# Optimization experiments

Hardware: AMD Instinct MI355X
Metric: run time of the kernel (lower is better)

The kernel has to match this reference:

```python
import jax, jax.numpy as jnp
import numpy as np

N, E, D, H = 50000, 800000, 128, 128
LN_EPS = 1e-3  # keras LayerNormalization default epsilon


def layer_norm(x, g, b):
    mu = jnp.mean(x, axis=-1, keepdims=True)
    var = jnp.mean(jnp.square(x - mu), axis=-1, keepdims=True)
    return (x - mu) * jax.lax.rsqrt(var + LN_EPS) * g + b


def mlp3(x, W1, b1, W2, b2, W3, b3, g1, be1, g2, be2):
    # 3-layer MLP: two hidden layers (relu + layernorm), linear output head
    h = layer_norm(jax.nn.relu(x @ W1 + b1), g1, be1)
    h = layer_norm(jax.nn.relu(h @ W2 + b2), g2, be2)
    return h @ W3 + b3


def _dense_init(key, fan_in, fan_out):
    return jax.random.normal(key, (fan_in, fan_out), jnp.float32) / np.sqrt(fan_in)


def setup_inputs() -> dict:
    key = jax.random.key(0)
    ks = jax.random.split(key, 12)
    query = jax.random.normal(ks[0], (N, D), jnp.float32)
    memory = jax.random.normal(ks[1], (N, D), jnp.float32)
    row = jnp.sort(jax.random.randint(ks[2], (E,), 0, N, jnp.int32))
    col = jax.random.randint(ks[3], (E,), 0, N, jnp.int32)
    # pre_process MLP: input 2D -> H -> H -> 1 (heads=1)
    pW1 = _dense_init(ks[4], 2 * D, H); pb1 = jnp.zeros((H,), jnp.float32)
    pW2 = _dense_init(ks[5], H, H);     pb2 = jnp.zeros((H,), jnp.float32)
    pW3 = _dense_init(ks[6], H, 1);     pb3 = jnp.zeros((1,), jnp.float32)
    pg1 = jnp.ones((H,), jnp.float32);  pbe1 = jnp.zeros((H,), jnp.float32)
    pg2 = jnp.ones((H,), jnp.float32);  pbe2 = jnp.zeros((H,), jnp.float32)
    # memory MLP: D -> H -> H -> H
    mW1 = _dense_init(ks[7], D, H); mb1 = jnp.zeros((H,), jnp.float32)
    mW2 = _dense_init(ks[8], H, H); mb2 = jnp.zeros((H,), jnp.float32)
    mW3 = _dense_init(ks[9], H, H); mb3 = jnp.zeros((H,), jnp.float32)
    mg1 = jnp.ones((H,), jnp.float32); mbe1 = jnp.zeros((H,), jnp.float32)
    mg2 = jnp.ones((H,), jnp.float32); mbe2 = jnp.zeros((H,), jnp.float32)
    return dict(query=query, memory=memory, row=row, col=col,
                pW1=pW1, pb1=pb1, pW2=pW2, pb2=pb2, pW3=pW3, pb3=pb3,
                pg1=pg1, pbe1=pbe1, pg2=pg2, pbe2=pbe2,
                mW1=mW1, mb1=mb1, mW2=mW2, mb2=mb2, mW3=mW3, mb3=mb3,
                mg1=mg1, mbe1=mbe1, mg2=mg2, mbe2=mbe2)


def reference(query, memory, row, col,
              pW1, pb1, pW2, pb2, pW3, pb3, pg1, pbe1, pg2, pbe2,
              mW1, mb1, mW2, mb2, mW3, mb3, mg1, mbe1, mg2, mbe2):
    # per-edge gather of query (target) and memory (source) node features
    units = jnp.concatenate([query[row], memory[col]], axis=-1)  # [E, 2D]
    h = jnp.tanh(mlp3(units, pW1, pb1, pW2, pb2, pW3, pb3, pg1, pbe1, pg2, pbe2))[:, 0]  # [E]
    mem_head = mlp3(memory, mW1, mb1, mW2, mb2, mW3, mb3, mg1, mbe1, mg2, mbe2)  # [N, H]
    # sparse_dense_matmul: out[i] = sum_{edges (i,j)} h_e * mem_head[j]
    out = jax.ops.segment_sum(h[:, None] * mem_head[col], row, num_segments=N)  # [N, H]
    return out
```

## Files before the change

kernel.cpp:

```cpp
#include <hip/hip_runtime.h>
#include <hip/hip_bf16.h>

typedef __attribute__((ext_vector_type(8))) short  svec8;
typedef __attribute__((ext_vector_type(4))) short  svec4;
typedef __attribute__((ext_vector_type(8))) __bf16 bfvec8;
typedef __attribute__((ext_vector_type(4))) float  f32x4;
typedef __attribute__((ext_vector_type(2))) float  f32x2;
typedef __attribute__((ext_vector_type(4))) unsigned uvec4;

#define LN_EPS 1e-3f

__device__ __forceinline__ short f2bf(float f) {
  union { float f; unsigned u; } v; v.f = f;
  unsigned u = v.u;
  u += 0x7fff + ((u >> 16) & 1);
  return (short)(u >> 16);
}

__device__ __forceinline__ unsigned pk2(float a, float b) {
  unsigned short ua = __builtin_bit_cast(unsigned short, (__bf16)a);
  unsigned short ub = __builtin_bit_cast(unsigned short, (__bf16)b);
  return (unsigned)ua | ((unsigned)ub << 16);
}

__device__ __forceinline__ f32x2 up2(unsigned w) {
  f32x2 r;
  r[0] = __builtin_bit_cast(float, w << 16);
  r[1] = __builtin_bit_cast(float, w & 0xffff0000u);
  return r;
}

__device__ __forceinline__ f32x4 mfma16(svec8 a, svec8 b, f32x4 c) {
  return __builtin_amdgcn_mfma_f32_16x16x32_bf16(
      __builtin_bit_cast(bfvec8, a), __builtin_bit_cast(bfvec8, b), c, 0, 0, 0);
}

__global__ __launch_bounds__(256) void setup_kernel(
    const float* __restrict__ pW1, const float* __restrict__ pW2,
    const float* __restrict__ pg1,
    const float* __restrict__ mW1, const float* __restrict__ mW2,
    const float* __restrict__ mW3,
    short* __restrict__ w1qp, short* __restrict__ w1mp,
    short* __restrict__ w2p,  short* __restrict__ mw1p,
    short* __restrict__ mw2p, short* __restrict__ mw3p,
    const int* __restrict__ row, int E, int N, int* __restrict__ off,
    const float* __restrict__ g1, const float* __restrict__ be1,
    const float* __restrict__ b2, const float* __restrict__ g2,
    const float* __restrict__ w3, const float* __restrict__ be2,
    const float* __restrict__ b3,
    float* __restrict__ s2, float* __restrict__ b2pv,
    float* __restrict__ gw, float* __restrict__ consts, int nboff)
{
  const int b = blockIdx.x;
  const int tid = threadIdx.x;
  if (b < 384) {
    int idx = b * 256 + tid;
    int which = idx >> 14, p = idx & 16383;
    int j = p & 7, lane = (p >> 3) & 63, t = p >> 9;
    int nf = t & 7, ks = t >> 3;
    int k = ks * 32 + (lane >> 4) * 8 + j;
    int n = nf * 16 + (lane & 15);
    const float* src; short* dst; float scale = 1.f;
    switch (which) {
      case 0:  src = pW1;         dst = w1qp; break;
      case 1:  src = pW1 + 16384; dst = w1mp; break;
      case 2:  src = pW2;         dst = w2p; scale = pg1[k]; break;
      case 3:  src = mW1;         dst = mw1p; break;
      case 4:  src = mW2;         dst = mw2p; break;
      default: src = mW3;         dst = mw3p; break;
    }
    dst[p] = f2bf(scale * src[k * 128 + n]);
  } else if (b < 384 + nboff) {
    int i = (b - 384) * 256 + tid;
    if (i > N) return;
    int lo = 0, hi = E;
    while (lo < hi) { int mid = (lo + hi) >> 1; if (row[mid] < i) lo = mid + 1; else hi = mid; }
    off[i] = lo;
  } else {
    __shared__ float tmp[256];
    int n = tid;
    if (n < 128) {
      float s = 0.f, bb = 0.f;
      for (int k = 0; k < 128; ++k) {
        float w = pW2[k * 128 + n];
        s  = fmaf(g1[k],  w, s);
        bb = fmaf(be1[k], w, bb);
      }
      s2[n]   = s;
      b2pv[n] = bb + b2[n];
      float g = g2[n] * w3[n];
      gw[n] = g;
      tmp[n]       = g;
      tmp[128 + n] = be2[n] * w3[n];
    }
    __syncthreads();
    if (n == 0) {
      float a = 0.f, c = 0.f;
      for (int i = 0; i < 128; ++i) { a += tmp[i]; c += tmp[128 + i]; }
      consts[0] = a;
      consts[1] = c + b3[0];
    }
  }
}

__global__ __launch_bounds__(256) void node_kernel(
    const float* __restrict__ mem, const float* __restrict__ query,
    const short* __restrict__ w1p, const short* __restrict__ w2p, const short* __restrict__ w3p,
    const short* __restrict__ wmp, const short* __restrict__ wqp,
    const float* __restrict__ b1v, const float* __restrict__ b2v, const float* __restrict__ b3v,
    const float* __restrict__ g1v, const float* __restrict__ be1v,
    const float* __restrict__ g2v, const float* __restrict__ be2v,
    const float* __restrict__ pb1,
    short* __restrict__ mhb, short* __restrict__ mwt, short* __restrict__ qwt,
    int N, int nbm)
{
  __shared__ short Xs[64 * 128];
  __shared__ short H1s[64 * 128];
  __shared__ float redA[4][64];
  __shared__ float redB[4][64];

  const int tid  = threadIdx.x;
  const int wv   = tid >> 6;
  const int lane = tid & 63;
  const int g16  = lane >> 4;
  const int l16  = lane & 15;
  const bool is_mem = (blockIdx.x < nbm);
  const int r0   = (is_mem ? blockIdx.x : blockIdx.x - nbm) * 64;
  const float* src = is_mem ? mem : query;

  #pragma unroll
  for (int it = 0; it < 8; ++it) {
    int c = tid + it * 256;
    int r = c >> 5;
    int part = c & 31;
    int gr = r0 + r; if (gr >= N) gr = N - 1;
    f32x4 v = *(const f32x4*)(src + (size_t)gr * 128 + part * 4);
    svec4 s;
    s[0] = f2bf(v[0]); s[1] = f2bf(v[1]); s[2] = f2bf(v[2]); s[3] = f2bf(v[3]);
    int b = (r * 256 + part * 8) ^ ((r & 7) << 4);
    *(svec4*)((char*)Xs + b) = s;
  }
  __syncthreads();

  const int nfb = wv * 2;
  const int col0 = wv * 32 + l16, col1 = col0 + 16;

  if (!is_mem) {
    f32x4 acc[4][2];
    #pragma unroll
    for (int mf = 0; mf < 4; ++mf) { f32x4 z = {0.f,0.f,0.f,0.f}; acc[mf][0] = z; acc[mf][1] = z; }
    #pragma unroll
    for (int ks = 0; ks < 4; ++ks) {
      svec8 bw0 = *(const svec8*)(wqp + (((ks * 8 + nfb + 0) * 64 + lane) << 3));
      svec8 bw1 = *(const svec8*)(wqp + (((ks * 8 + nfb + 1) * 64 + lane) << 3));
      #pragma unroll
      for (int mf = 0; mf < 4; ++mf) {
        int row = mf * 16 + l16;
        int byt = (row * 256 + ks * 64 + g16 * 16) ^ ((row & 7) << 4);
        svec8 a = *(const svec8*)((const char*)Xs + byt);
        acc[mf][0] = mfma16(a, bw0, acc[mf][0]);
        acc[mf][1] = mfma16(a, bw1, acc[mf][1]);
      }
    }
    float bi0 = pb1[col0], bi1 = pb1[col1];
    #pragma unroll
    for (int mf = 0; mf < 4; ++mf)
      #pragma unroll
      for (int r = 0; r < 4; ++r) {
        int rr = mf * 16 + g16 * 4 + r;
        int gr = r0 + rr;
        if (gr < N) {
          qwt[(size_t)gr * 128 + col0] = f2bf(acc[mf][0][r] + bi0);
          qwt[(size_t)gr * 128 + col1] = f2bf(acc[mf][1][r] + bi1);
        }
      }
    return;
  }

  f32x4 acc[4][2], accm[4][2];
  #pragma unroll
  for (int mf = 0; mf < 4; ++mf) {
    f32x4 z = {0.f,0.f,0.f,0.f};
    acc[mf][0] = z; acc[mf][1] = z; accm[mf][0] = z; accm[mf][1] = z;
  }
  #pragma unroll
  for (int ks = 0; ks < 4; ++ks) {
    svec8 bw0 = *(const svec8*)(w1p + (((ks * 8 + nfb + 0) * 64 + lane) << 3));
    svec8 bw1 = *(const svec8*)(w1p + (((ks * 8 + nfb + 1) * 64 + lane) << 3));
    svec8 bm0 = *(const svec8*)(wmp + (((ks * 8 + nfb + 0) * 64 + lane) << 3));
    svec8 bm1 = *(const svec8*)(wmp + (((ks * 8 + nfb + 1) * 64 + lane) << 3));
    #pragma unroll
    for (int mf = 0; mf < 4; ++mf) {
      int row = mf * 16 + l16;
      int byt = (row * 256 + ks * 64 + g16 * 16) ^ ((row & 7) << 4);
      svec8 a = *(const svec8*)((const char*)Xs + byt);
      acc[mf][0]  = mfma16(a, bw0, acc[mf][0]);
      acc[mf][1]  = mfma16(a, bw1, acc[mf][1]);
      accm[mf][0] = mfma16(a, bm0, accm[mf][0]);
      accm[mf][1] = mfma16(a, bm1, accm[mf][1]);
    }
  }
  #pragma unroll
  for (int mf = 0; mf < 4; ++mf)
    #pragma unroll
    for (int r = 0; r < 4; ++r) {
      int rr = mf * 16 + g16 * 4 + r;
      int gr = r0 + rr;
      if (gr < N) {
        mwt[(size_t)gr * 128 + col0] = f2bf(accm[mf][0][r]);
        mwt[(size_t)gr * 128 + col1] = f2bf(accm[mf][1][r]);
      }
    }

  float bi0 = b1v[col0], bi1 = b1v[col1];
  float ga0 = g1v[col0], ga1 = g1v[col1];
  float bb0 = be1v[col0], bb1 = be1v[col1];
  float y[4][2][4], ps[4][4], pq[4][4];
  #pragma unroll
  for (int mf = 0; mf < 4; ++mf)
    #pragma unroll
    for (int r = 0; r < 4; ++r) {
      float y0 = fmaxf(acc[mf][0][r] + bi0, 0.f);
      float y1 = fmaxf(acc[mf][1][r] + bi1, 0.f);
      y[mf][0][r] = y0; y[mf][1][r] = y1;
      ps[mf][r] = y0 + y1;
      pq[mf][r] = y0 * y0 + y1 * y1;
    }
  #pragma unroll
  for (int mk = 1; mk <= 8; mk <<= 1)
    #pragma unroll
    for (int mf = 0; mf < 4; ++mf)
      #pragma unroll
      for (int r = 0; r < 4; ++r) {
        ps[mf][r] += __shfl_xor(ps[mf][r], mk, 64);
        pq[mf][r] += __shfl_xor(pq[mf][r], mk, 64);
      }
  if (l16 == 0) {
    #pragma unroll
    for (int mf = 0; mf < 4; ++mf)
      #pragma unroll
      for (int r = 0; r < 4; ++r) {
        redA[wv][mf * 16 + g16 * 4 + r] = ps[mf][r];
        redB[wv][mf * 16 + g16 * 4 + r] = pq[mf][r];
      }
  }
  __syncthreads();
  #pragma unroll
  for (int mf = 0; mf < 4; ++mf)
    #pragma unroll
    for (int r = 0; r < 4; ++r) {
      int rr = mf * 16 + g16 * 4 + r;
      float s = redA[0][rr] + redA[1][rr] + redA[2][rr] + redA[3][rr];
      float q = redB[0][rr] + redB[1][rr] + redB[2][rr] + redB[3][rr];
      float mu = s * (1.f / 128.f);
      float var = fmaxf(q * (1.f / 128.f) - mu * mu, 0.f);
      float rstd = rsqrtf(var + LN_EPS);
      float z0 = (y[mf][0][r] - mu) * rstd * ga0 + bb0;
      float z1 = (y[mf][1][r] - mu) * rstd * ga1 + bb1;
      int by0 = (rr * 256 + col0 * 2) ^ ((rr & 7) << 4);
      int by1 = (rr * 256 + col1 * 2) ^ ((rr & 7) << 4);
      *(short*)((char*)H1s + by0) = f2bf(z0);
      *(short*)((char*)H1s + by1) = f2bf(z1);
    }
  __syncthreads();

  f32x4 acc2[4][2];
  #pragma unroll
  for (int mf = 0; mf < 4; ++mf) { f32x4 z = {0.f,0.f,0.f,0.f}; acc2[mf][0] = z; acc2[mf][1] = z; }
  #pragma unroll
  for (int ks = 0; ks < 4; ++ks) {
    svec8 bw0 = *(const svec8*)(w2p + (((ks * 8 + nfb + 0) * 64 + lane) << 3));
    svec8 bw1 = *(const svec8*)(w2p + (((ks * 8 + nfb + 1) * 64 + lane) << 3));
    #pragma unroll
    for (int mf = 0; mf < 4; ++mf) {
      int row = mf * 16 + l16;
      int byt = (row * 256 + ks * 64 + g16 * 16) ^ ((row & 7) << 4);
      svec8 a = *(const svec8*)((const char*)H1s + byt);
      acc2[mf][0] = mfma16(a, bw0, acc2[mf][0]);
      acc2[mf][1] = mfma16(a, bw1, acc2[mf][1]);
    }
  }

  float bi20 = b2v[col0], bi21 = b2v[col1];
  float ga20 = g2v[col0], ga21 = g2v[col1];
  float bb20 = be2v[col0], bb21 = be2v[col1];
  float y2[4][2][4];
  #pragma unroll
  for (int mf = 0; mf < 4; ++mf)
    #pragma unroll
    for (int r = 0; r < 4; ++r) {
      float y0 = fmaxf(acc2[mf][0][r] + bi20, 0.f);
      float y1 = fmaxf(acc2[mf][1][r] + bi21, 0.f);
      y2[mf][0][r] = y0; y2[mf][1][r] = y1;
      ps[mf][r] = y0 + y1;
      pq[mf][r] = y0 * y0 + y1 * y1;
    }
  #pragma unroll
  for (int mk = 1; mk <= 8; mk <<= 1)
    #pragma unroll
    for (int mf = 0; mf < 4; ++mf)
      #pragma unroll
      for (int r = 0; r < 4; ++r) {
        ps[mf][r] += __shfl_xor(ps[mf][r], mk, 64);
        pq[mf][r] += __shfl_xor(pq[mf][r], mk, 64);
      }
  if (l16 == 0) {
    #pragma unroll
    for (int mf = 0; mf < 4; ++mf)
      #pragma unroll
      for (int r = 0; r < 4; ++r) {
        redA[wv][mf * 16 + g16 * 4 + r] = ps[mf][r];
        redB[wv][mf * 16 + g16 * 4 + r] = pq[mf][r];
      }
  }
  __syncthreads();
  #pragma unroll
  for (int mf = 0; mf < 4; ++mf)
    #pragma unroll
    for (int r = 0; r < 4; ++r) {
      int rr = mf * 16 + g16 * 4 + r;
      float s = redA[0][rr] + redA[1][rr] + redA[2][rr] + redA[3][rr];
      float q = redB[0][rr] + redB[1][rr] + redB[2][rr] + redB[3][rr];
      float mu = s * (1.f / 128.f);
      float var = fmaxf(q * (1.f / 128.f) - mu * mu, 0.f);
      float rstd = rsqrtf(var + LN_EPS);
      float z0 = (y2[mf][0][r] - mu) * rstd * ga20 + bb20;
      float z1 = (y2[mf][1][r] - mu) * rstd * ga21 + bb21;
      int by0 = (rr * 256 + col0 * 2) ^ ((rr & 7) << 4);
      int by1 = (rr * 256 + col1 * 2) ^ ((rr & 7) << 4);
      *(short*)((char*)Xs + by0) = f2bf(z0);
      *(short*)((char*)Xs + by1) = f2bf(z1);
    }
  __syncthreads();

  f32x4 acc3[4][2];
  #pragma unroll
  for (int mf = 0; mf < 4; ++mf) { f32x4 z = {0.f,0.f,0.f,0.f}; acc3[mf][0] = z; acc3[mf][1] = z; }
  #pragma unroll
  for (int ks = 0; ks < 4; ++ks) {
    svec8 bw0 = *(const svec8*)(w3p + (((ks * 8 + nfb + 0) * 64 + lane) << 3));
    svec8 bw1 = *(const svec8*)(w3p + (((ks * 8 + nfb + 1) * 64 + lane) << 3));
    #pragma unroll
    for (int mf = 0; mf < 4; ++mf) {
      int row = mf * 16 + l16;
      int byt = (row * 256 + ks * 64 + g16 * 16) ^ ((row & 7) << 4);
      svec8 a = *(const svec8*)((const char*)Xs + byt);
      acc3[mf][0] = mfma16(a, bw0, acc3[mf][0]);
      acc3[mf][1] = mfma16(a, bw1, acc3[mf][1]);
    }
  }
  float bi30 = b3v[col0], bi31 = b3v[col1];
  #pragma unroll
  for (int mf = 0; mf < 4; ++mf)
    #pragma unroll
    for (int r = 0; r < 4; ++r) {
      int rr = mf * 16 + g16 * 4 + r;
      int gr = r0 + rr;
      if (gr < N) {
        mhb[(size_t)gr * 128 + col0] = f2bf(acc3[mf][0][r] + bi30);
        mhb[(size_t)gr * 128 + col1] = f2bf(acc3[mf][1][r] + bi31);
      }
    }
}

__device__ __forceinline__ void relu_stats(const svec8* qv, const svec8* mv,
                                           svec8* yf, float& ps_o, float& pq_o) {
  f32x2 psv = {0.f, 0.f}, pqv = {0.f, 0.f};
  #pragma unroll
  for (int ks2 = 0; ks2 < 4; ++ks2) {
    uvec4 qu = __builtin_bit_cast(uvec4, qv[ks2]);
    uvec4 mu = __builtin_bit_cast(uvec4, mv[ks2]);
    uvec4 u;
    #pragma unroll
    for (int p = 0; p < 4; ++p) {
      f32x2 y = __builtin_elementwise_max(up2(qu[p]) + up2(mu[p]), (f32x2){0.f, 0.f});
      psv += y;
      pqv += y * y;
      u[p] = pk2(y[0], y[1]);
    }
    yf[ks2] = __builtin_bit_cast(svec8, u);
  }
  float ps = psv[0] + psv[1], pq = pqv[0] + pqv[1];
  ps += __shfl_xor(ps, 16, 64); pq += __shfl_xor(pq, 16, 64);
  ps += __shfl_xor(ps, 32, 64); pq += __shfl_xor(pq, 32, 64);
  ps_o = ps; pq_o = pq;
}

__device__ __forceinline__ void epilogue(const f32x4* acc2, float rstd1, float mu1,
    const float* s2v, const float* b2pv, const float* gwv, float Sgw, float cb,
    float* __restrict__ hout, int e, bool valid, int lane, int g) {
  f32x2 rst = {rstd1, rstd1};
  f32x2 nmu = {-rstd1 * mu1, -rstd1 * mu1};
  f32x2 psv = {0.f,0.f}, pqv = {0.f,0.f}, pwv = {0.f,0.f};
  #pragma unroll
  for (int nf = 0; nf < 8; ++nf) {
    f32x4 s2 = *(const f32x4*)(s2v  + nf * 16 + g * 4);
    f32x4 bb = *(const f32x4*)(b2pv + nf * 16 + g * 4);
    f32x4 gw = *(const f32x4*)(gwv  + nf * 16 + g * 4);
    #pragma unroll
    for (int p = 0; p < 2; ++p) {
      f32x2 a   = { acc2[nf][2*p], acc2[nf][2*p+1] };
      f32x2 s2p = { s2[2*p], s2[2*p+1] };
      f32x2 bbp = { bb[2*p], bb[2*p+1] };
      f32x2 gwp = { gw[2*p], gw[2*p+1] };
      f32x2 h = rst * a + (nmu * s2p + bbp);
      f32x2 y = __builtin_elementwise_max(h, (f32x2){0.f, 0.f});
      psv += y;
      pqv += y * y;
      pwv += y * gwp;
    }
  }
  float ps2 = psv[0] + psv[1], pq2 = pqv[0] + pqv[1], pw2 = pwv[0] + pwv[1];
  ps2 += __shfl_xor(ps2, 16, 64); pq2 += __shfl_xor(pq2, 16, 64); pw2 += __shfl_xor(pw2, 16, 64);
  ps2 += __shfl_xor(ps2, 32, 64); pq2 += __shfl_xor(pq2, 32, 64); pw2 += __shfl_xor(pw2, 32, 64);
  float mu2   = ps2 * (1.f / 128.f);
  float var2  = fmaxf(pq2 * (1.f / 128.f) - mu2 * mu2, 0.f);
  float rstd2 = rsqrtf(var2 + LN_EPS);
  float p3 = fmaf(rstd2, pw2 - mu2 * Sgw, cb);
  if (lane < 16 && valid) hout[e] = tanhf(p3);
}

__global__ __launch_bounds__(256, 3) void edge_mlp_kernel(
    const short* __restrict__ qwt, const short* __restrict__ mwt,
    const int* __restrict__ rowi, const int* __restrict__ coli,
    const short* __restrict__ w2p,
    const float* __restrict__ s2v, const float* __restrict__ b2pv,
    const float* __restrict__ gwv, const float* __restrict__ consts,
    float* __restrict__ hout, int E)
{
  __shared__ short w2s[16384];

  const int tid  = threadIdx.x;
  const int wv   = tid >> 6;
  const int lane = tid & 63;
  const int g    = lane >> 4;
  const int l16  = lane & 15;

  const int nb  = gridDim.x;
  const int q8  = nb >> 3, r8 = nb & 7;
  const int xcd = blockIdx.x & 7, sub = blockIdx.x >> 3;
  const int bid = (xcd < r8 ? xcd * (q8 + 1) : r8 * (q8 + 1) + (xcd - r8) * q8) + sub;

  #pragma unroll
  for (int it = 0; it < 8; ++it) {
    int o = (it * 256 + tid) * 8;
    *(f32x4*)(w2s + o) = *(const f32x4*)(w2p + o);
  }
  __syncthreads();

  const int eb = bid * 128 + wv * 32;
  const int e0 = eb + l16, e1 = eb + 16 + l16;
  const bool v0 = (e0 < E), v1 = (e1 < E);
  const int ee0 = v0 ? e0 : 0, ee1 = v1 ? e1 : 0;
  const short* q0 = qwt + (size_t)rowi[ee0] * 128 + g * 8;
  const short* m0 = mwt + (size_t)coli[ee0] * 128 + g * 8;
  const short* q1 = qwt + (size_t)rowi[ee1] * 128 + g * 8;
  const short* m1 = mwt + (size_t)coli[ee1] * 128 + g * 8;

  svec8 qv0[4], mv0[4], qv1[4], mv1[4];
  #pragma unroll
  for (int ks2 = 0; ks2 < 4; ++ks2) {
    qv0[ks2] = *(const svec8*)(q0 + ks2 * 32);
    mv0[ks2] = *(const svec8*)(m0 + ks2 * 32);
    qv1[ks2] = *(const svec8*)(q1 + ks2 * 32);
    mv1[ks2] = *(const svec8*)(m1 + ks2 * 32);
  }

  svec8 yf0[4], yf1[4];
  float ps0, pq0, ps1, pq1;
  relu_stats(qv0, mv0, yf0, ps0, pq0);
  relu_stats(qv1, mv1, yf1, ps1, pq1);
  float mu1_0   = ps0 * (1.f / 128.f);
  float rstd1_0 = rsqrtf(fmaxf(pq0 * (1.f / 128.f) - mu1_0 * mu1_0, 0.f) + LN_EPS);
  float mu1_1   = ps1 * (1.f / 128.f);
  float rstd1_1 = rsqrtf(fmaxf(pq1 * (1.f / 128.f) - mu1_1 * mu1_1, 0.f) + LN_EPS);

  f32x4 acc2a[8], acc2b[8];
  #pragma unroll
  for (int nf = 0; nf < 8; ++nf) { f32x4 z = {0.f,0.f,0.f,0.f}; acc2a[nf] = z; acc2b[nf] = z; }
  __builtin_amdgcn_s_setprio(1);
  #pragma unroll
  for (int ks2 = 0; ks2 < 4; ++ks2) {
    #pragma unroll
    for (int nf = 0; nf < 8; ++nf) {
      svec8 w = *(const svec8*)(w2s + (((ks2 * 8 + nf) * 64 + lane) << 3));
      acc2a[nf] = mfma16(w, yf0[ks2], acc2a[nf]);
      acc2b[nf] = mfma16(w, yf1[ks2], acc2b[nf]);
    }
  }
  __builtin_amdgcn_s_setprio(0);

  float Sgw = consts[0], cb = consts[1];
  epilogue(acc2a, rstd1_0, mu1_0, s2v, b2pv, gwv, Sgw, cb, hout, e0, v0, lane, g);
  epilogue(acc2b, rstd1_1, mu1_1, s2v, b2pv, gwv, Sgw, cb, hout, e1, v1, lane, g);
}

__global__ __launch_bounds__(256) void segsum_kernel(
    const int* __restrict__ off, const int* __restrict__ coli,
    const float* __restrict__ hbuf, const short* __restrict__ mhb,
    float* __restrict__ out, int N)
{
  int wv = threadIdx.x >> 6, lane = threadIdx.x & 63;
  int i = blockIdx.x * 4 + wv;
  if (i >= N) return;
  int s = __builtin_amdgcn_readfirstlane(off[i]);
  int e = __builtin_amdgcn_readfirstlane(off[i + 1]);
  f32x2 acc = {0.f, 0.f};
  int k = s;
  for (; k + 8 <= e; k += 8) {
    float h[8]; unsigned w[8];
    #pragma unroll
    for (int u = 0; u < 8; ++u) {
      h[u] = hbuf[k + u];
      w[u] = *(const unsigned*)(mhb + (size_t)coli[k + u] * 128 + lane * 2);
    }
    #pragma unroll
    for (int u = 0; u < 8; ++u)
      acc += (f32x2){h[u], h[u]} * up2(w[u]);
  }
  for (; k < e; ++k) {
    float h = hbuf[k];
    unsigned w = *(const unsigned*)(mhb + (size_t)coli[k] * 128 + lane * 2);
    acc += (f32x2){h, h} * up2(w);
  }
  *(f32x2*)(out + (size_t)i * 128 + lane * 2) = acc;
}

extern "C" void kernel_launch(void* const* d_in, const int* in_sizes, int n_in,
                              void* d_out, int out_size, void* d_ws, size_t ws_size,
                              hipStream_t stream) {
  const float* query = (const float*)d_in[0];
  const float* mem   = (const float*)d_in[1];
  const int*   row   = (const int*)d_in[2];
  const int*   col   = (const int*)d_in[3];
  const float* pW1 = (const float*)d_in[4];  const float* pb1 = (const float*)d_in[5];
  const float* pW2 = (const float*)d_in[6];  const float* pb2 = (const float*)d_in[7];
  const float* pW3 = (const float*)d_in[8];  const float* pb3 = (const float*)d_in[9];
  const float* pg1 = (const float*)d_in[10]; const float* pbe1 = (const float*)d_in[11];
  const float* pg2 = (const float*)d_in[12]; const float* pbe2 = (const float*)d_in[13];
  const float* mW1 = (const float*)d_in[14]; const float* mb1 = (const float*)d_in[15];
  const float* mW2 = (const float*)d_in[16]; const float* mb2 = (const float*)d_in[17];
  const float* mW3 = (const float*)d_in[18]; const float* mb3 = (const float*)d_in[19];
  const float* mg1 = (const float*)d_in[20]; const float* mbe1 = (const float*)d_in[21];
  const float* mg2 = (const float*)d_in[22]; const float* mbe2 = (const float*)d_in[23];

  const int N = in_sizes[0] / 128;
  const int E = in_sizes[2];

  char* ws = (char*)d_ws;
  short* w1qp = (short*)(ws + 0);
  short* w1mp = (short*)(ws + 32768);
  short* w2p  = (short*)(ws + 65536);
  short* mw1p = (short*)(ws + 98304);
  short* mw2p = (short*)(ws + 131072);
  short* mw3p = (short*)(ws + 163840);
  float* s2v  = (float*)(ws + 196608);
  float* b2pv = (float*)(ws + 197120);
  float* gwv  = (float*)(ws + 197632);
  float* cons = (float*)(ws + 198144);
  int*   offs = (int*)(ws + 198208);
  size_t o = 198208 + (((size_t)(N + 1) * 4 + 255) / 256) * 256;
  short* qwt  = (short*)(ws + o);  o += (size_t)N * 128 * 2;
  short* mwt  = (short*)(ws + o);  o += (size_t)N * 128 * 2;
  short* mhb  = (short*)(ws + o);  o += (size_t)N * 128 * 2;
  float* hbuf = (float*)(ws + o);  o += (size_t)E * 4;

  if (ws_size < o) return;

  const int nboff = (N + 1 + 255) / 256;
  setup_kernel<<<384 + nboff + 1, 256, 0, stream>>>(
      pW1, pW2, pg1, mW1, mW2, mW3, w1qp, w1mp, w2p, mw1p, mw2p, mw3p,
      row, E, N, offs,
      pg1, pbe1, pb2, pg2, pW3, pbe2, pb3, s2v, b2pv, gwv, cons, nboff);

  const int nbm = (N + 63) / 64;
  node_kernel<<<2 * nbm, 256, 0, stream>>>(
      mem, query, mw1p, mw2p, mw3p, w1mp, w1qp,
      mb1, mb2, mb3, mg1, mbe1, mg2, mbe2, pb1,
      mhb, mwt, qwt, N, nbm);

  edge_mlp_kernel<<<(E + 127) / 128, 256, 0, stream>>>(
      qwt, mwt, row, col, w2p, s2v, b2pv, gwv, cons, hbuf, E);

  segsum_kernel<<<(N + 3) / 4, 256, 0, stream>>>(offs, col, hbuf, mhb, (float*)d_out, N);
}
```

Baseline: 179.0 us.

## Give each wave a private 16-row tile in the node MLP kernel

The node MLP kernel now has each wave own 16 full rows across all 128 output columns, instead of four waves sharing a 64-row tile split by columns. Inputs are loaded straight from global memory into MFMA A-fragments, and LayerNorm statistics are reduced entirely with in-wave shuffles. This removes the shared staging tile, the cross-wave reduction arrays and every __syncthreads. In exchange, each wave now loads the full weight matrices itself, which raises weight traffic from cache, and it holds more accumulators in registers.

```diff
diff --git a/kernel.cpp b/kernel.cpp
--- a/kernel.cpp
+++ b/kernel.cpp
@@ -114,253 +114,185 @@
     short* __restrict__ mhb, short* __restrict__ mwt, short* __restrict__ qwt,
     int N, int nbm)
 {
-  __shared__ short Xs[64 * 128];
-  __shared__ short H1s[64 * 128];
-  __shared__ float redA[4][64];
-  __shared__ float redB[4][64];
+  __shared__ char Hs[4][4096];
 
   const int tid  = threadIdx.x;
   const int wv   = tid >> 6;
   const int lane = tid & 63;
-  const int g16  = lane >> 4;
+  const int g    = lane >> 4;
   const int l16  = lane & 15;
   const bool is_mem = (blockIdx.x < nbm);
-  const int r0   = (is_mem ? blockIdx.x : blockIdx.x - nbm) * 64;
+  const int r0   = (is_mem ? blockIdx.x : blockIdx.x - nbm) * 64 + wv * 16;
   const float* src = is_mem ? mem : query;
 
-  #pragma unroll
-  for (int it = 0; it < 8; ++it) {
-    int c = tid + it * 256;
-    int r = c >> 5;
-    int part = c & 31;
-    int gr = r0 + r; if (gr >= N) gr = N - 1;
-    f32x4 v = *(const f32x4*)(src + (size_t)gr * 128 + part * 4);
-    svec4 s;
-    s[0] = f2bf(v[0]); s[1] = f2bf(v[1]); s[2] = f2bf(v[2]); s[3] = f2bf(v[3]);
-    int b = (r * 256 + part * 8) ^ ((r & 7) << 4);
-    *(svec4*)((char*)Xs + b) = s;
-  }
-  __syncthreads();
-
-  const int nfb = wv * 2;
-  const int col0 = wv * 32 + l16, col1 = col0 + 16;
+  int grow = r0 + l16; if (grow >= N) grow = N - 1;
+  const float* xrow = src + (size_t)grow * 128 + g * 8;
+  svec8 xf[4];
+  #pragma unroll
+  for (int ks = 0; ks < 4; ++ks) {
+    f32x4 a = *(const f32x4*)(xrow + ks * 32);
+    f32x4 b = *(const f32x4*)(xrow + ks * 32 + 4);
+    uvec4 u;
+    u[0] = pk2(a[0], a[1]); u[1] = pk2(a[2], a[3]);
+    u[2] = pk2(b[0], b[1]); u[3] = pk2(b[2], b[3]);
+    xf[ks] = __builtin_bit_cast(svec8, u);
+  }
 
   if (!is_mem) {
-    f32x4 acc[4][2];
-    #pragma unroll
-    for (int mf = 0; mf < 4; ++mf) { f32x4 z = {0.f,0.f,0.f,0.f}; acc[mf][0] = z; acc[mf][1] = z; }
-    #pragma unroll
-    for (int ks = 0; ks < 4; ++ks) {
-      svec8 bw0 = *(const svec8*)(wqp + (((ks * 8 + nfb + 0) * 64 + lane) << 3));
-      svec8 bw1 = *(const svec8*)(wqp + (((ks * 8 + nfb + 1) * 64 + lane) << 3));
+    f32x4 acc[8];
+    #pragma unroll
+    for (int nf = 0; nf < 8; ++nf) { f32x4 z = {0.f,0.f,0.f,0.f}; acc[nf] = z; }
+    #pragma unroll
+    for (int ks = 0; ks < 4; ++ks)
       #pragma unroll
-      for (int mf = 0; mf < 4; ++mf) {
-        int row = mf * 16 + l16;
-        int byt = (row * 256 + ks * 64 + g16 * 16) ^ ((row & 7) << 4);
-        svec8 a = *(const svec8*)((const char*)Xs + byt);
-        acc[mf][0] = mfma16(a, bw0, acc[mf][0]);
-        acc[mf][1] = mfma16(a, bw1, acc[mf][1]);
+      for (int nf = 0; nf < 8; ++nf) {
+        svec8 bw = *(const svec8*)(wqp + (((ks * 8 + nf) * 64 + lane) << 3));
+        acc[nf] = mfma16(xf[ks], bw, acc[nf]);
       }
-    }
-    float bi0 = pb1[col0], bi1 = pb1[col1];
-    #pragma unroll
-    for (int mf = 0; mf < 4; ++mf)
+    #pragma unroll
+    for (int nf = 0; nf < 8; ++nf) {
+      float bi = pb1[nf * 16 + l16];
       #pragma unroll
       for (int r = 0; r < 4; ++r) {
-        int rr = mf * 16 + g16 * 4 + r;
-        int gr = r0 + rr;
-        if (gr < N) {
-          qwt[(size_t)gr * 128 + col0] = f2bf(acc[mf][0][r] + bi0);
-          qwt[(size_t)gr * 128 + col1] = f2bf(acc[mf][1][r] + bi1);
-        }
+        int gr = r0 + g * 4 + r;
+        if (gr < N) qwt[(size_t)gr * 128 + nf * 16 + l16] = f2bf(acc[nf][r] + bi);
       }
+    }
     return;
   }
 
-  f32x4 acc[4][2], accm[4][2];
-  #pragma unroll
-  for (int mf = 0; mf < 4; ++mf) {
-    f32x4 z = {0.f,0.f,0.f,0.f};
-    acc[mf][0] = z; acc[mf][1] = z; accm[mf][0] = z; accm[mf][1] = z;
-  }
+  f32x4 acc[8], accm[8];
+  #pragma unroll
+  for (int nf = 0; nf < 8; ++nf) { f32x4 z = {0.f,0.f,0.f,0.f}; acc[nf] = z; accm[nf] = z; }
+  #pragma unroll
+  for (int ks = 0; ks < 4; ++ks)
+    #pragma unroll
+    for (int nf = 0; nf < 8; ++nf) {
+      svec8 bw = *(const svec8*)(w1p + (((ks * 8 + nf) * 64 + lane) << 3));
+      svec8 bm = *(const svec8*)(wmp + (((ks * 8 + nf) * 64 + lane) << 3));
+      acc[nf]  = mfma16(xf[ks], bw, acc[nf]);
+      accm[nf] = mfma16(xf[ks], bm, accm[nf]);
+    }
+  #pragma unroll
+  for (int nf = 0; nf < 8; ++nf)
+    #pragma unroll
+    for (int r = 0; r < 4; ++r) {
+      int gr = r0 + g * 4 + r;
+      if (gr < N) mwt[(size_t)gr * 128 + nf * 16 + l16] = f2bf(accm[nf][r]);
+    }
+
+  char* slice = Hs[wv];
+
+  float ps[4] = {0,0,0,0}, pq[4] = {0,0,0,0};
+  #pragma unroll
+  for (int nf = 0; nf < 8; ++nf) {
+    float bi = b1v[nf * 16 + l16];
+    #pragma unroll
+    for (int r = 0; r < 4; ++r) {
+      float y = fmaxf(acc[nf][r] + bi, 0.f);
+      acc[nf][r] = y;
+      ps[r] += y;
+      pq[r] = fmaf(y, y, pq[r]);
+    }
+  }
+  #pragma unroll
+  for (int mk = 1; mk <= 8; mk <<= 1)
+    #pragma unroll
+    for (int r = 0; r < 4; ++r) {
+      ps[r] += __shfl_xor(ps[r], mk, 64);
+      pq[r] += __shfl_xor(pq[r], mk, 64);
+    }
+  #pragma unroll
+  for (int r = 0; r < 4; ++r) {
+    float mu = ps[r] * (1.f / 128.f);
+    float var = fmaxf(pq[r] * (1.f / 128.f) - mu * mu, 0.f);
+    float rstd = rsqrtf(var + LN_EPS);
+    int rloc = g * 4 + r;
+    #pragma unroll
+    for (int nf = 0; nf < 8; ++nf) {
+      float ga = g1v[nf * 16 + l16], bb = be1v[nf * 16 + l16];
+      float z = (acc[nf][r] - mu) * rstd * ga + bb;
+      int byt = (rloc * 256 + (nf * 16 + l16) * 2) ^ ((rloc & 7) << 4);
+      *(short*)(slice + byt) = f2bf(z);
+    }
+  }
+
+  svec8 hf[4];
   #pragma unroll
   for (int ks = 0; ks < 4; ++ks) {
-    svec8 bw0 = *(const svec8*)(w1p + (((ks * 8 + nfb + 0) * 64 + lane) << 3));
-    svec8 bw1 = *(const svec8*)(w1p + (((ks * 8 + nfb + 1) * 64 + lane) << 3));
-    svec8 bm0 = *(const svec8*)(wmp + (((ks * 8 + nfb + 0) * 64 + lane) << 3));
-    svec8 bm1 = *(const svec8*)(wmp + (((ks * 8 + nfb + 1) * 64 + lane) << 3));
-    #pragma unroll
-    for (int mf = 0; mf < 4; ++mf) {
-      int row = mf * 16 + l16;
-      int byt = (row * 256 + ks * 64 + g16 * 16) ^ ((row & 7) << 4);
-      svec8 a = *(const svec8*)((const char*)Xs + byt);
-      acc[mf][0]  = mfma16(a, bw0, acc[mf][0]);
-      acc[mf][1]  = mfma16(a, bw1, acc[mf][1]);
-      accm[mf][0] = mfma16(a, bm0, accm[mf][0]);
-      accm[mf][1] = mfma16(a, bm1, accm[mf][1]);
-    }
-  }
-  #pragma unroll
-  for (int mf = 0; mf < 4; ++mf)
+    int byt = (l16 * 256 + (ks * 32 + g * 8) * 2) ^ ((l16 & 7) << 4);
+    hf[ks] = *(const svec8*)(slice + byt);
+  }
+  f32x4 acc2[8];
+  #pragma unroll
+  for (int nf = 0; nf < 8; ++nf) { f32x4 z = {0.f,0.f,0.f,0.f}; acc2[nf] = z; }
+  #pragma unroll
+  for (int ks = 0; ks < 4; ++ks)
+    #pragma unroll
+    for (int nf = 0; nf < 8; ++nf) {
+      svec8 bw = *(const svec8*)(w2p + (((ks * 8 + nf) * 64 + lane) << 3));
+      acc2[nf] = mfma16(hf[ks], bw, acc2[nf]);
+    }
+
+  #pragma unroll
+  for (int r = 0; r < 4; ++r) { ps[r] = 0.f; pq[r] = 0.f; }
+  #pragma unroll
+  for (int nf = 0; nf < 8; ++nf) {
+    float bi = b2v[nf * 16 + l16];
     #pragma unroll
     for (int r = 0; r < 4; ++r) {
-      int rr = mf * 16 + g16 * 4 + r;
-      int gr = r0 + rr;
-      if (gr < N) {
-        mwt[(size_t)gr * 128 + col0] = f2bf(accm[mf][0][r]);
-        mwt[(size_t)gr * 128 + col1] = f2bf(accm[mf][1][r]);
-      }
-    }
-
-  float bi0 = b1v[col0], bi1 = b1v[col1];
-  float ga0 = g1v[col0], ga1 = g1v[col1];
-  float bb0 = be1v[col0], bb1 = be1v[col1];
-  float y[4][2][4], ps[4][4], pq[4][4];
-  #pragma unroll
-  for (int mf = 0; mf < 4; ++mf)
+      float y = fmaxf(acc2[nf][r] + bi, 0.f);
+      acc2[nf][r] = y;
+      ps[r] += y;
+      pq[r] = fmaf(y, y, pq[r]);
+    }
+  }
+  #pragma unroll
+  for (int mk = 1; mk <= 8; mk <<= 1)
     #pragma unroll
     for (int r = 0; r < 4; ++r) {
-      float y0 = fmaxf(acc[mf][0][r] + bi0, 0.f);
-      float y1 = fmaxf(acc[mf][1][r] + bi1, 0.f);
-      y[mf][0][r] = y0; y[mf][1][r] = y1;
-      ps[mf][r] = y0 + y1;
-      pq[mf][r] = y0 * y0 + y1 * y1;
-    }
-  #pragma unroll
-  for (int mk = 1; mk <= 8; mk <<= 1)
-    #pragma unroll
-    for (int mf = 0; mf < 4; ++mf)
-      #pragma unroll
-      for (int r = 0; r < 4; ++r) {
-        ps[mf][r] += __shfl_xor(ps[mf][r], mk, 64);
-        pq[mf][r] += __shfl_xor(pq[mf][r], mk, 64);
-      }
-  if (l16 == 0) {
-    #pragma unroll
-    for (int mf = 0; mf < 4; ++mf)
-      #pragma unroll
-      for (int r = 0; r < 4; ++r) {
-        redA[wv][mf * 16 + g16 * 4 + r] = ps[mf][r];
-        redB[wv][mf * 16 + g16 * 4 + r] = pq[mf][r];
-      }
-  }
-  __syncthreads();
-  #pragma unroll
-  for (int mf = 0; mf < 4; ++mf)
+      ps[r] += __shfl_xor(ps[r], mk, 64);
+      pq[r] += __shfl_xor(pq[r], mk, 64);
+    }
+  #pragma unroll
+  for (int r = 0; r < 4; ++r) {
+    float mu = ps[r] * (1.f / 128.f);
+    float var = fmaxf(pq[r] * (1.f / 128.f) - mu * mu, 0.f);
+    float rstd = rsqrtf(var + LN_EPS);
+    int rloc = g * 4 + r;
+    #pragma unroll
+    for (int nf = 0; nf < 8; ++nf) {
+      float ga = g2v[nf * 16 + l16], bb = be2v[nf * 16 + l16];
+      float z = (acc2[nf][r] - mu) * rstd * ga + bb;
+      int byt = (rloc * 256 + (nf * 16 + l16) * 2) ^ ((rloc & 7) << 4);
+      *(short*)(slice + byt) = f2bf(z);
+    }
+  }
+
+  #pragma unroll
+  for (int ks = 0; ks < 4; ++ks) {
+    int byt = (l16 * 256 + (ks * 32 + g * 8) * 2) ^ ((l16 & 7) << 4);
+    hf[ks] = *(const svec8*)(slice + byt);
+  }
+  f32x4 acc3[8];
+  #pragma unroll
+  for (int nf = 0; nf < 8; ++nf) { f32x4 z = {0.f,0.f,0.f,0.f}; acc3[nf] = z; }
+  #pragma unroll
+  for (int ks = 0; ks < 4; ++ks)
+    #pragma unroll
+    for (int nf = 0; nf < 8; ++nf) {
+      svec8 bw = *(const svec8*)(w3p + (((ks * 8 + nf) * 64 + lane) << 3));
+      acc3[nf] = mfma16(hf[ks], bw, acc3[nf]);
+    }
+  #pragma unroll
+  for (int nf = 0; nf < 8; ++nf) {
+    float bi = b3v[nf * 16 + l16];
     #pragma unroll
     for (int r = 0; r < 4; ++r) {
-      int rr = mf * 16 + g16 * 4 + r;
-      float s = redA[0][rr] + redA[1][rr] + redA[2][rr] + redA[3][rr];
-      float q = redB[0][rr] + redB[1][rr] + redB[2][rr] + redB[3][rr];
-      float mu = s * (1.f / 128.f);
-      float var = fmaxf(q * (1.f / 128.f) - mu * mu, 0.f);
-      float rstd = rsqrtf(var + LN_EPS);
-      float z0 = (y[mf][0][r] - mu) * rstd * ga0 + bb0;
-      float z1 = (y[mf][1][r] - mu) * rstd * ga1 + bb1;
-      int by0 = (rr * 256 + col0 * 2) ^ ((rr & 7) << 4);
-      int by1 = (rr * 256 + col1 * 2) ^ ((rr & 7) << 4);
-      *(short*)((char*)H1s + by0) = f2bf(z0);
-      *(short*)((char*)H1s + by1) = f2bf(z1);
-    }
-  __syncthreads();
-
-  f32x4 acc2[4][2];
-  #pragma unroll
-  for (int mf = 0; mf < 4; ++mf) { f32x4 z = {0.f,0.f,0.f,0.f}; acc2[mf][0] = z; acc2[mf][1] = z; }
-  #pragma unroll
-  for (int ks = 0; ks < 4; ++ks) {
-    svec8 bw0 = *(const svec8*)(w2p + (((ks * 8 + nfb + 0) * 64 + lane) << 3));
-    svec8 bw1 = *(const svec8*)(w2p + (((ks * 8 + nfb + 1) * 64 + lane) << 3));
-    #pragma unroll
-    for (int mf = 0; mf < 4; ++mf) {
-      int row = mf * 16 + l16;
-      int byt = (row * 256 + ks * 64 + g16 * 16) ^ ((row & 7) << 4);
-      svec8 a = *(const svec8*)((const char*)H1s + byt);
-      acc2[mf][0] = mfma16(a, bw0, acc2[mf][0]);
-      acc2[mf][1] = mfma16(a, bw1, acc2[mf][1]);
-    }
-  }
-
-  float bi20 = b2v[col0], bi21 = b2v[col1];
-  float ga20 = g2v[col0], ga21 = g2v[col1];
-  float bb20 = be2v[col0], bb21 = be2v[col1];
-  float y2[4][2][4];
-  #pragma unroll
-  for (int mf = 0; mf < 4; ++mf)
-    #pragma unroll
-    for (int r = 0; r < 4; ++r) {
-      float y0 = fmaxf(acc2[mf][0][r] + bi20, 0.f);
-      float y1 = fmaxf(acc2[mf][1][r] + bi21, 0.f);
-      y2[mf][0][r] = y0; y2[mf][1][r] = y1;
-      ps[mf][r] = y0 + y1;
-      pq[mf][r] = y0 * y0 + y1 * y1;
-    }
-  #pragma unroll
-  for (int mk = 1; mk <= 8; mk <<= 1)
-    #pragma unroll
-    for (int mf = 0; mf < 4; ++mf)
-      #pragma unroll
-      for (int r = 0; r < 4; ++r) {
-        ps[mf][r] += __shfl_xor(ps[mf][r], mk, 64);
-        pq[mf][r] += __shfl_xor(pq[mf][r], mk, 64);
-      }
-  if (l16 == 0) {
-    #pragma unroll
-    for (int mf = 0; mf < 4; ++mf)
-      #pragma unroll
-      for (int r = 0; r < 4; ++r) {
-        redA[wv][mf * 16 + g16 * 4 + r] = ps[mf][r];
-        redB[wv][mf * 16 + g16 * 4 + r] = pq[mf][r];
-      }
-  }
-  __syncthreads();
-  #pragma unroll
-  for (int mf = 0; mf < 4; ++mf)
-    #pragma unroll
-    for (int r = 0; r < 4; ++r) {
-      int rr = mf * 16 + g16 * 4 + r;
-      float s = redA[0][rr] + redA[1][rr] + redA[2][rr] + redA[3][rr];
-      float q = redB[0][rr] + redB[1][rr] + redB[2][rr] + redB[3][rr];
-      float mu = s * (1.f / 128.f);
-      float var = fmaxf(q * (1.f / 128.f) - mu * mu, 0.f);
-      float rstd = rsqrtf(var + LN_EPS);
-      float z0 = (y2[mf][0][r] - mu) * rstd * ga20 + bb20;
-      float z1 = (y2[mf][1][r] - mu) * rstd * ga21 + bb21;
-      int by0 = (rr * 256 + col0 * 2) ^ ((rr & 7) << 4);
-      int by1 = (rr * 256 + col1 * 2) ^ ((rr & 7) << 4);
-      *(short*)((char*)Xs + by0) = f2bf(z0);
-      *(short*)((char*)Xs + by1) = f2bf(z1);
-    }
-  __syncthreads();
-
-  f32x4 acc3[4][2];
-  #pragma unroll
-  for (int mf = 0; mf < 4; ++mf) { f32x4 z = {0.f,0.f,0.f,0.f}; acc3[mf][0] = z; acc3[mf][1] = z; }
-  #pragma unroll
-  for (int ks = 0; ks < 4; ++ks) {
-    svec8 bw0 = *(const svec8*)(w3p + (((ks * 8 + nfb + 0) * 64 + lane) << 3));
-    svec8 bw1 = *(const svec8*)(w3p + (((ks * 8 + nfb + 1) * 64 + lane) << 3));
-    #pragma unroll
-    for (int mf = 0; mf < 4; ++mf) {
-      int row = mf * 16 + l16;
-      int byt = (row * 256 + ks * 64 + g16 * 16) ^ ((row & 7) << 4);
-      svec8 a = *(const svec8*)((const char*)Xs + byt);
-      acc3[mf][0] = mfma16(a, bw0, acc3[mf][0]);
-      acc3[mf][1] = mfma16(a, bw1, acc3[mf][1]);
-    }
-  }
-  float bi30 = b3v[col0], bi31 = b3v[col1];
-  #pragma unroll
-  for (int mf = 0; mf < 4; ++mf)
-    #pragma unroll
-    for (int r = 0; r < 4; ++r) {
-      int rr = mf * 16 + g16 * 4 + r;
-      int gr = r0 + rr;
-      if (gr < N) {
-        mhb[(size_t)gr * 128 + col0] = f2bf(acc3[mf][0][r] + bi30);
-        mhb[(size_t)gr * 128 + col1] = f2bf(acc3[mf][1][r] + bi31);
-      }
-    }
+      int gr = r0 + g * 4 + r;
+      if (gr < N) mhb[(size_t)gr * 128 + nf * 16 + l16] = f2bf(acc3[nf][r] + bi);
+    }
+  }
 }
 
 __device__ __forceinline__ void relu_stats(const svec8* qv, const svec8* mv,
```

After: 171.7 us. 1.04x faster.
